# Kernel tuning notes

Measured on AMD Instinct MI355X. Metric: run time of the kernel, lower is better.

## Reference

```python
import jax, jax.numpy as jnp
import numpy as np

DIM = 256
NUM_HEADS = 8
HEAD_DIM = 64
NUM_MEM_KV = 4
HIDDEN = NUM_HEADS * HEAD_DIM  # 512


def rmsnorm(x, g):
    # F.normalize(x, dim=1) * g * sqrt(C)
    c = x.shape[1]
    n = jnp.sqrt(jnp.sum(x * x, axis=1, keepdims=True))
    xn = x / jnp.maximum(n, 1e-12)
    return xn * g * (c ** 0.5)


def setup_inputs() -> dict:
    key = jax.random.key(0)
    ks = jax.random.split(key, 7)
    b, h, w = 16, 64, 64
    x = jax.random.normal(ks[0], (b, DIM, h, w), dtype=jnp.float32)
    g_in = jnp.ones((1, DIM, 1, 1), dtype=jnp.float32)
    w_qkv = jax.random.normal(ks[1], (HIDDEN * 3, DIM), dtype=jnp.float32) * (1.0 / np.sqrt(DIM))
    mem_kv = jax.random.normal(ks[2], (2, NUM_HEADS, HEAD_DIM, NUM_MEM_KV), dtype=jnp.float32)
    w_out = jax.random.normal(ks[3], (DIM, HIDDEN), dtype=jnp.float32) * (1.0 / np.sqrt(HIDDEN))
    b_out = jax.random.normal(ks[4], (DIM,), dtype=jnp.float32) * 0.01
    g_out = jnp.ones((1, DIM, 1, 1), dtype=jnp.float32)
    return {"x": x, "g_in": g_in, "w_qkv": w_qkv, "mem_kv": mem_kv,
            "w_out": w_out, "b_out": b_out, "g_out": g_out}


def reference(x, g_in, w_qkv, mem_kv, w_out, b_out, g_out):
    b, c, h, w = x.shape
    scale = HEAD_DIM ** (-0.5)
    xn = rmsnorm(x, g_in)
    # 1x1 conv (no bias) as GEMM: [b, 3*hidden, h, w]
    qkv = jnp.einsum('bcxy,oc->boxy', xn, w_qkv)
    q, k, v = jnp.split(qkv, 3, axis=1)
    # b (heads d) x y -> b heads d n
    def to_heads(t):
        return t.reshape(b, NUM_HEADS, HEAD_DIM, h * w)
    q, k, v = to_heads(q), to_heads(k), to_heads(v)
    mem_k = jnp.broadcast_to(mem_kv[0], (b, NUM_HEADS, HEAD_DIM, NUM_MEM_KV))
    mem_v = jnp.broadcast_to(mem_kv[1], (b, NUM_HEADS, HEAD_DIM, NUM_MEM_KV))
    k = jnp.concatenate([mem_k, k], axis=-1)
    v = jnp.concatenate([mem_v, v], axis=-1)
    q = jax.nn.softmax(q, axis=-2) * scale   # softmax over head_dim
    k = jax.nn.softmax(k, axis=-1)           # softmax over sequence
    context = jnp.einsum('bhdn,bhen->bhde', k, v)  # [b,h,d,d] per-head context
    out = jnp.einsum('bhde,bhdn->bhen', context, q)  # [b,h,d,n]
    out = out.reshape(b, HIDDEN, h, w)
    out = jnp.einsum('bcxy,oc->boxy', out, w_out) + b_out[None, :, None, None]
    return rmsnorm(out, g_out)
```

## Files before the change

kernel.cpp:

```cpp
#include <hip/hip_runtime.h>
#include <hip/hip_bf16.h>

typedef __hip_bfloat16 bf16;
typedef short bf16x8 __attribute__((ext_vector_type(8)));
typedef float f32x4 __attribute__((ext_vector_type(4)));

#define PTOT  65536
#define NPOS  4096
#define CIN   256
#define HID   512
#define HD    64

__device__ __forceinline__ float us2f(unsigned short u) {
    return __uint_as_float(((unsigned int)u) << 16);
}
__device__ __forceinline__ float ldf(const void* p, size_t i, bool bf) {
    return bf ? us2f(((const unsigned short*)p)[i]) : ((const float*)p)[i];
}
__device__ __forceinline__ unsigned short f2bs(float v) {
    __hip_bfloat16 h = __float2bfloat16(v);
    return *reinterpret_cast<unsigned short*>(&h);
}
__device__ __forceinline__ void gld16(const void* g, void* s) {
    __builtin_amdgcn_global_load_lds(
        (const __attribute__((address_space(1))) unsigned int*)g,
        (__attribute__((address_space(3))) unsigned int*)s, 16, 0, 0);
}

__global__ __launch_bounds__(256) void k_detect(const unsigned* __restrict__ x,
                                                int* __restrict__ flag) {
    int t = threadIdx.x;
    unsigned w = x[(size_t)t * 997];
    unsigned e7 = (w >> 8) & 0x7f;
    __shared__ int s[256];
    s[t] = (e7 >= 58 && e7 <= 66) ? 1 : 0;
    __syncthreads();
    for (int k = 128; k > 0; k >>= 1) { if (t < k) s[t] += s[t + k]; __syncthreads(); }
    if (t == 0) flag[0] = (s[0] >= 128) ? 1 : 0;
}

__global__ void k_relay(const int* __restrict__ src, int* __restrict__ dst) {
    dst[0] = src[0];
}

__global__ __launch_bounds__(256) void k_cvt(const void* __restrict__ src,
        unsigned short* __restrict__ dst, int n, const int* __restrict__ flag) {
    bool bf = flag[0] != 0;
    int i = blockIdx.x * 256 + threadIdx.x;
    if (i < n) dst[i] = f2bs(ldf(src, i, bf));
}

template<bool BF>
__device__ __forceinline__ void norm_xn_body(const void* __restrict__ x,
        const void* __restrict__ g, unsigned short* __restrict__ xn,
        float* __restrict__ smem)
{
    float* xs   = smem;
    float* gS   = smem + 17216;
    float* red2 = smem + 17472;
    float* sS   = smem + 18496;
    const int t = threadIdx.x;
    const int p0 = blockIdx.x * 64;
    const int b = p0 >> 12;
    const int posbase = p0 & 4095;
    gS[t] = ldf(g, t, BF);
    __syncthreads();
    const int pl4 = (t & 15) * 4;
    const int crow = t >> 4;
    const size_t xbase = ((size_t)b * CIN) << 12;
    float ssq[4] = {0.f, 0.f, 0.f, 0.f};
    #pragma unroll
    for (int rr = 0; rr < 16; ++rr) {
        int c = rr * 16 + crow;
        float v[4];
        if (BF) {
            ushort4 u = *(const ushort4*)((const unsigned short*)x + xbase +
                                          ((size_t)c << 12) + posbase + pl4);
            v[0] = us2f(u.x); v[1] = us2f(u.y); v[2] = us2f(u.z); v[3] = us2f(u.w);
        } else {
            float4 f = *(const float4*)((const float*)x + xbase +
                                        ((size_t)c << 12) + posbase + pl4);
            v[0] = f.x; v[1] = f.y; v[2] = f.z; v[3] = f.w;
        }
        float gv = gS[c];
        float* row = xs + (c >> 6) * 4304 + (c & 63) * 67;
        #pragma unroll
        for (int e = 0; e < 4; ++e) {
            ssq[e] += v[e] * v[e];
            row[pl4 + e] = v[e] * gv;
        }
    }
    #pragma unroll
    for (int e = 0; e < 4; ++e) red2[crow * 64 + pl4 + e] = ssq[e];
    __syncthreads();
    if (t < 64) {
        float tot = 0.f;
        #pragma unroll
        for (int j = 0; j < 16; ++j) tot += red2[j * 64 + t];
        sS[t] = 16.0f / fmaxf(sqrtf(tot), 1e-12f);
    }
    __syncthreads();
    const int pr = t >> 2, c0 = (t & 3) * 64;
    const float sc = sS[pr];
    const float* base = xs + (t & 3) * 4304 + pr;
    unsigned short* dst = &xn[(size_t)(p0 + pr) * 256 + c0];
    #pragma unroll
    for (int q = 0; q < 4; ++q) {
        unsigned short tmp[16];
        #pragma unroll
        for (int j = 0; j < 16; ++j)
            tmp[j] = f2bs(base[(q * 16 + j) * 67] * sc);
        *(uint4*)(dst + q * 16)     = ((uint4*)tmp)[0];
        *(uint4*)(dst + q * 16 + 8) = ((uint4*)tmp)[1];
    }
}
__global__ __launch_bounds__(256) void k_norm_xn(
        const void* __restrict__ x, const void* __restrict__ g,
        unsigned short* __restrict__ xn, const int* __restrict__ flag)
{
    __shared__ float smem[18560];
    if (flag[0]) norm_xn_body<true>(x, g, xn, smem);
    else         norm_xn_body<false>(x, g, xn, smem);
}

template<int KTOT, bool BIAS, int OSTRIDE>
__global__ __launch_bounds__(256) void k_mfma(
        const bf16* __restrict__ Am, const bf16* __restrict__ Bm,
        const void* __restrict__ bias, bf16* __restrict__ C,
        const int* __restrict__ flag)
{
    __shared__ __align__(16) unsigned short As[128 * 32];
    __shared__ __align__(16) unsigned short Bs[128 * 32];
    const int tid = threadIdx.x;
    const int wv = tid >> 6, lane = tid & 63;
    const int quad = lane >> 4, l16 = lane & 15;
    const int wm = wv >> 1, wn = wv & 1;
    const int m0 = blockIdx.y * 128, n0 = blockIdx.x * 128;
    f32x4 acc[4][4] = {};
    const bf16* gA = Am + (size_t)(m0 + (tid >> 2)) * KTOT + (tid & 3) * 8;
    const bf16* gB = Bm + (size_t)(n0 + (tid >> 2)) * KTOT + (tid & 3) * 8;
    unsigned short* lA = As + wv * 512;
    unsigned short* lB = Bs + wv * 512;
    for (int k0 = 0; k0 < KTOT; k0 += 32) {
        gld16(gA + k0, lA);
        gld16(gA + (size_t)64 * KTOT + k0, lA + 2048);
        gld16(gB + k0, lB);
        gld16(gB + (size_t)64 * KTOT + k0, lB + 2048);
        __syncthreads();
        bf16x8 bfr[4];
        #pragma unroll
        for (int j = 0; j < 4; ++j)
            bfr[j] = *(const bf16x8*)&Bs[(wn * 64 + j * 16 + l16) * 32 + quad * 8];
        #pragma unroll
        for (int i = 0; i < 4; ++i) {
            bf16x8 af = *(const bf16x8*)&As[(wm * 64 + i * 16 + l16) * 32 + quad * 8];
            #pragma unroll
            for (int j = 0; j < 4; ++j)
                acc[i][j] = __builtin_amdgcn_mfma_f32_16x16x32_bf16(af, bfr[j], acc[i][j], 0, 0, 0);
        }
        __syncthreads();
    }
    bool bf = BIAS ? (flag[0] != 0) : false;
    #pragma unroll
    for (int i = 0; i < 4; ++i) {
        int row = m0 + wm * 64 + i * 16 + quad * 4;
        #pragma unroll
        for (int r = 0; r < 4; ++r) {
            float bv = BIAS ? ldf(bias, row + r, bf) : 0.0f;
            #pragma unroll
            for (int j = 0; j < 4; ++j) {
                int col = n0 + wn * 64 + j * 16 + l16;
                C[(size_t)(row + r) * OSTRIDE + col] = __float2bfloat16(acc[i][j][r] + bv);
            }
        }
    }
}

__global__ __launch_bounds__(512) void k_kvgemm(
        const bf16* __restrict__ Am, const bf16* __restrict__ Bm,
        bf16* __restrict__ C)
{
    __shared__ __align__(16) unsigned short As[128 * 256];
    __shared__ __align__(16) unsigned short Bs[2][64 * 256];
    const int t = threadIdx.x;
    const int w = t >> 6, lane = t & 63;
    const int quad = lane >> 4, l16 = lane & 15;
    const int wm = w >> 1, wn = w & 1;
    const int p = blockIdx.x;
    const int xcd = p & 7, slot = p >> 3;
    const int chunk = xcd * 4 + (slot & 3);
    const int mt = slot >> 2;
    const int m0 = mt * 128;
    const size_t cbase = (size_t)chunk * 2048;

    const int srow = t >> 5;
    const int sks  = (t & 31) ^ (srow & 7);

    #pragma unroll
    for (int q = 0; q < 8; ++q)
        gld16(Am + (size_t)(m0 + q * 16 + srow) * 256 + sks * 8,
              (char*)As + q * 8192 + w * 1024);
    #pragma unroll
    for (int q = 0; q < 4; ++q)
        gld16(Bm + (cbase + q * 16 + srow) * 256 + sks * 8,
              (char*)Bs[0] + q * 8192 + w * 1024);
    #pragma unroll
    for (int q = 0; q < 4; ++q)
        gld16(Bm + (cbase + 64 + q * 16 + srow) * 256 + sks * 8,
              (char*)Bs[1] + q * 8192 + w * 1024);

    asm volatile("s_waitcnt vmcnt(8)" ::: "memory");
    __builtin_amdgcn_s_barrier();
    asm volatile("" ::: "memory");

    bf16x8 af[2][8];
    #pragma unroll
    for (int i = 0; i < 2; ++i) {
        int row = wm * 32 + i * 16 + l16;
        #pragma unroll
        for (int kk = 0; kk < 8; ++kk)
            af[i][kk] = *(const bf16x8*)((const char*)As + row * 512 +
                         (((kk * 4 + quad) ^ (row & 7)) << 4));
    }

    for (int s = 0; s < 32; ++s) {
        if (s > 0) {
            asm volatile("" ::: "memory");
            __builtin_amdgcn_s_barrier();
            asm volatile("" ::: "memory");
            if (s + 1 < 32) {
                #pragma unroll
                for (int q = 0; q < 4; ++q)
                    gld16(Bm + (cbase + (size_t)(s + 1) * 64 + q * 16 + srow) * 256 + sks * 8,
                          (char*)Bs[(s + 1) & 1] + q * 8192 + w * 1024);
            }
        }
        if (s == 0)      asm volatile("s_waitcnt vmcnt(4)"  ::: "memory");
        else if (s < 31) asm volatile("s_waitcnt vmcnt(20)" ::: "memory");
        else             asm volatile("s_waitcnt vmcnt(16)" ::: "memory");
        __builtin_amdgcn_s_barrier();
        asm volatile("" ::: "memory");

        const unsigned short* Bbuf = Bs[s & 1];
        f32x4 acc[2][2] = {};
        #pragma unroll
        for (int kk = 0; kk < 8; ++kk) {
            bf16x8 bfr[2];
            #pragma unroll
            for (int j = 0; j < 2; ++j) {
                int row = wn * 32 + j * 16 + l16;
                bfr[j] = *(const bf16x8*)((const char*)Bbuf + row * 512 +
                          (((kk * 4 + quad) ^ (row & 7)) << 4));
            }
            #pragma unroll
            for (int i = 0; i < 2; ++i)
                #pragma unroll
                for (int j = 0; j < 2; ++j)
                    acc[i][j] = __builtin_amdgcn_mfma_f32_16x16x32_bf16(af[i][kk], bfr[j], acc[i][j], 0, 0, 0);
        }
        #pragma unroll
        for (int i = 0; i < 2; ++i) {
            #pragma unroll
            for (int r = 0; r < 4; ++r) {
                int row = m0 + wm * 32 + i * 16 + quad * 4 + r;
                size_t col = cbase + (size_t)s * 64 + wn * 32;
                #pragma unroll
                for (int j = 0; j < 2; ++j)
                    C[(size_t)row * PTOT + col + j * 16 + l16] = __float2bfloat16(acc[i][j][r]);
            }
        }
    }
}

__global__ __launch_bounds__(512, 2) void k_qapply(
        const bf16* __restrict__ xn, const bf16* __restrict__ wq,
        const unsigned short* __restrict__ ct_bf,
        unsigned short* __restrict__ oat_pe)
{
    __shared__ __align__(16) char smem[163840];
    const int t = threadIdx.x;
    const int w = t >> 6, lane = t & 63;
    const int quad = lane >> 4, l16 = lane & 15;
    const int wm = w >> 1, wn = w & 1;
    const int bid = blockIdx.x;
    const int hp = (bid >> 3) & 3;
    const int c  = (bid & 7) | ((bid >> 5) << 3);
    const int n0 = hp * 128;
    const size_t P0 = (size_t)c * 1024;
    const int b = c >> 2;
    const int srow = t >> 5, sks = (t & 31) ^ (srow & 7);

    #pragma unroll
    for (int k = 0; k < 2; ++k) {
        int u = k * 512 + t;
        int hh = u >> 9, rem = u & 511, e = rem >> 3, sl = rem & 7;
        gld16(ct_bf + (size_t)(b * 8 + hp * 2 + hh) * 4096 + e * 64 + ((sl ^ (e & 7)) * 8),
              smem + 81920 + k * 8192 + w * 1024);
    }
    #pragma unroll
    for (int q = 0; q < 8; ++q)
        gld16(wq + (size_t)(n0 + q * 16 + srow) * 256 + sks * 8,
              smem + q * 8192 + w * 1024);
    #pragma unroll
    for (int q = 0; q < 4; ++q)
        gld16(xn + (P0 + q * 16 + srow) * 256 + sks * 8,
              smem + 98304 + q * 8192 + w * 1024);
    #pragma unroll
    for (int q = 0; q < 4; ++q)
        gld16(xn + (P0 + 64 + q * 16 + srow) * 256 + sks * 8,
              smem + 131072 + q * 8192 + w * 1024);

    asm volatile("s_waitcnt vmcnt(8)" ::: "memory");
    __builtin_amdgcn_s_barrier();
    asm volatile("" ::: "memory");

    bf16x8 wqf[4][8];
    #pragma unroll
    for (int j = 0; j < 4; ++j) {
        int row = wn * 64 + j * 16 + l16;
        #pragma unroll
        for (int kk = 0; kk < 8; ++kk)
            wqf[j][kk] = *(const bf16x8*)(smem + row * 512 +
                          (((kk * 4 + quad) ^ (row & 7)) << 4));
    }

    unsigned short* qsm = (unsigned short*)(smem + 65536);

    for (int s = 0; s < 16; ++s) {
        if (s > 0) {
            asm volatile("" ::: "memory");
            __builtin_amdgcn_s_barrier();
            asm volatile("" ::: "memory");
            if (s + 1 < 16) {
                #pragma unroll
                for (int q = 0; q < 4; ++q)
                    gld16(xn + (P0 + (size_t)(s + 1) * 64 + q * 16 + srow) * 256 + sks * 8,
                          smem + 98304 + ((s + 1) & 1) * 32768 + q * 8192 + w * 1024);
            }
        }
        if (s == 0)      asm volatile("s_waitcnt vmcnt(4)"  ::: "memory");
        else if (s < 15) asm volatile("s_waitcnt vmcnt(20)" ::: "memory");
        else             asm volatile("s_waitcnt vmcnt(16)" ::: "memory");
        __builtin_amdgcn_s_barrier();
        asm volatile("" ::: "memory");

        const char* Bbuf = smem + 98304 + (s & 1) * 32768;
        f32x4 acc[4] = {};
        #pragma unroll
        for (int kk = 0; kk < 8; ++kk) {
            int row = wm * 16 + l16;
            bf16x8 xf = *(const bf16x8*)(Bbuf + row * 512 +
                          (((kk * 4 + quad) ^ (row & 7)) << 4));
            #pragma unroll
            for (int j = 0; j < 4; ++j)
                acc[j] = __builtin_amdgcn_mfma_f32_16x16x32_bf16(xf, wqf[j][kk], acc[j], 0, 0, 0);
        }

        #pragma unroll
        for (int r = 0; r < 4; ++r) {
            float m = fmaxf(fmaxf(acc[0][r], acc[1][r]), fmaxf(acc[2][r], acc[3][r]));
            m = fmaxf(m, __shfl_xor(m, 1));
            m = fmaxf(m, __shfl_xor(m, 2));
            m = fmaxf(m, __shfl_xor(m, 4));
            m = fmaxf(m, __shfl_xor(m, 8));
            float ev[4], sum = 0.f;
            #pragma unroll
            for (int j = 0; j < 4; ++j) { ev[j] = __expf(acc[j][r] - m); sum += ev[j]; }
            sum += __shfl_xor(sum, 1);
            sum += __shfl_xor(sum, 2);
            sum += __shfl_xor(sum, 4);
            sum += __shfl_xor(sum, 8);
            float inv = 0.125f / sum;
            int pos = wm * 16 + quad * 4 + r;
            #pragma unroll
            for (int j = 0; j < 4; ++j) {
                int ch = wn * 64 + j * 16 + l16;
                qsm[pos * 128 + (((ch >> 3) ^ (pos & 7)) << 3) + (ch & 7)] = f2bs(ev[j] * inv);
            }
        }

        f32x4 acc2[4] = {};
        #pragma unroll
        for (int kk = 0; kk < 2; ++kk) {
            int row = wm * 16 + l16;
            bf16x8 qf = *(const bf16x8*)(smem + 65536 + row * 256 +
                         (((wn * 8 + kk * 4 + quad) ^ (row & 7)) << 4));
            #pragma unroll
            for (int j = 0; j < 4; ++j) {
                int e = j * 16 + l16;
                bf16x8 cf = *(const bf16x8*)(smem + 81920 + wn * 8192 + e * 128 +
                             (((kk * 4 + quad) ^ (e & 7)) << 4));
                acc2[j] = __builtin_amdgcn_mfma_f32_16x16x32_bf16(qf, cf, acc2[j], 0, 0, 0);
            }
        }
        #pragma unroll
        for (int j = 0; j < 4; ++j)
            #pragma unroll
            for (int r = 0; r < 4; ++r) {
                size_t prow = P0 + (size_t)s * 64 + wm * 16 + quad * 4 + r;
                oat_pe[prow * HID + n0 + wn * 64 + j * 16 + l16] = f2bs(acc2[j][r]);
            }
    }
}

__global__ __launch_bounds__(256) void k_kstats(
        const bf16* __restrict__ kv, const void* __restrict__ memkv,
        float* __restrict__ rowmax, float* __restrict__ rowinv,
        const int* __restrict__ flag)
{
    bool bf = flag[0] != 0;
    int r = blockIdx.x;
    int b = r >> 9, hd = r & 511;
    const unsigned short* krow = (const unsigned short*)kv + (size_t)hd * PTOT + b * NPOS;
    int t = threadIdx.x;
    float vals[16];
    float m = -1e30f;
    #pragma unroll
    for (int i = 0; i < 16; ++i) {
        vals[i] = us2f(krow[t + (i << 8)]);
        m = fmaxf(m, vals[i]);
    }
    float mv = (t < 4) ? ldf(memkv, hd * 4 + t, bf) : -1e30f;
    m = fmaxf(m, mv);
    __shared__ float red[256];
    red[t] = m; __syncthreads();
    for (int s = 128; s > 0; s >>= 1) {
        if (t < s) red[t] = fmaxf(red[t], red[t + s]);
        __syncthreads();
    }
    float M = red[0]; __syncthreads();
    float sum = 0.f;
    #pragma unroll
    for (int i = 0; i < 16; ++i) sum += __expf(vals[i] - M);
    if (t < 4) sum += __expf(mv - M);
    red[t] = sum; __syncthreads();
    for (int s = 128; s > 0; s >>= 1) {
        if (t < s) red[t] += red[t + s];
        __syncthreads();
    }
    if (t == 0) { rowmax[r] = M; rowinv[r] = 1.0f / red[0]; }
}

__global__ __launch_bounds__(256) void k_context_mfma(
        const bf16* __restrict__ kv, const void* __restrict__ memkv,
        const float* __restrict__ rowmax, const float* __restrict__ rowinv,
        float* __restrict__ ctpart, const int* __restrict__ flag)
{
    bool bf = flag[0] != 0;
    int bh = blockIdx.x, chunk = blockIdx.y;
    int b = bh >> 3, h = bh & 7;
    __shared__ __align__(16) unsigned short As[4][64 * 32];
    __shared__ __align__(16) unsigned short Bs[4][64 * 32];
    __shared__ float rmS[64], riS[64];
    const int tid = threadIdx.x;
    if (tid < 64) {
        rmS[tid] = rowmax[(b << 9) + (h << 6) + tid];
        riS[tid] = rowinv[(b << 9) + (h << 6) + tid];
    }
    __syncthreads();
    const int wv = tid >> 6, lane = tid & 63;
    const int quad = lane >> 4, l16 = lane & 15;
    const int wm = wv >> 1, wn = wv & 1;
    const int krow = tid >> 2, kseg = tid & 3;
    const float rm = rmS[krow], ri = riS[krow];
    const unsigned short* kbase = (const unsigned short*)kv + (size_t)(h * HD) * PTOT + b * NPOS + chunk * 1024;
    const unsigned short* vbase = (const unsigned short*)kv + (size_t)(HID + h * HD) * PTOT + b * NPOS + chunk * 1024;
    f32x4 acc[2][2] = {};
    for (int s = 0; s < 8; ++s) {
        int nb = s * 128;
        #pragma unroll
        for (int kk = 0; kk < 4; ++kk) {
            uint4 u = *(const uint4*)(kbase + (size_t)krow * PTOT + nb + kk * 32 + kseg * 8);
            unsigned short out[8];
            const unsigned short* us = (const unsigned short*)&u;
            #pragma unroll
            for (int e = 0; e < 8; ++e)
                out[e] = f2bs(__expf(us2f(us[e]) - rm) * ri);
            *(uint4*)&As[kk][krow * 32 + kseg * 8] = *(uint4*)out;
        }
        #pragma unroll
        for (int kk = 0; kk < 4; ++kk)
            gld16(vbase + (size_t)(wv * 16 + (lane >> 2)) * PTOT + nb + kk * 32 + (lane & 3) * 8,
                  &Bs[kk][wv * 512]);
        __syncthreads();
        #pragma unroll
        for (int kk = 0; kk < 4; ++kk) {
            bf16x8 bfr[2];
            #pragma unroll
            for (int j = 0; j < 2; ++j)
                bfr[j] = *(const bf16x8*)&Bs[kk][(wn * 32 + j * 16 + l16) * 32 + quad * 8];
            #pragma unroll
            for (int i = 0; i < 2; ++i) {
                bf16x8 af = *(const bf16x8*)&As[kk][(wm * 32 + i * 16 + l16) * 32 + quad * 8];
                #pragma unroll
                for (int j = 0; j < 2; ++j)
                    acc[i][j] = __builtin_amdgcn_mfma_f32_16x16x32_bf16(af, bfr[j], acc[i][j], 0, 0, 0);
            }
        }
        __syncthreads();
    }
    if (chunk == 0) {
        float mv[2][4];
        #pragma unroll
        for (int j = 0; j < 2; ++j) {
            int e = wn * 32 + j * 16 + l16;
            #pragma unroll
            for (int mm = 0; mm < 4; ++mm)
                mv[j][mm] = ldf(memkv, 2048 + ((h << 6) + e) * 4 + mm, bf);
        }
        #pragma unroll
        for (int i = 0; i < 2; ++i) {
            #pragma unroll
            for (int r = 0; r < 4; ++r) {
                int d = wm * 32 + i * 16 + quad * 4 + r;
                #pragma unroll
                for (int mm = 0; mm < 4; ++mm) {
                    float kw = __expf(ldf(memkv, ((h << 6) + d) * 4 + mm, bf) - rmS[d]) * riS[d];
                    #pragma unroll
                    for (int j = 0; j < 2; ++j)
                        acc[i][j][r] = fmaf(kw, mv[j][mm], acc[i][j][r]);
                }
            }
        }
    }
    float* outp = ctpart + (size_t)(chunk * 128 + bh) * 4096;
    #pragma unroll
    for (int i = 0; i < 2; ++i) {
        #pragma unroll
        for (int r = 0; r < 4; ++r) {
            int d = wm * 32 + i * 16 + quad * 4 + r;
            #pragma unroll
            for (int j = 0; j < 2; ++j) {
                int e = wn * 32 + j * 16 + l16;
                outp[d * 64 + e] = acc[i][j][r];
            }
        }
    }
}

__global__ __launch_bounds__(256) void k_ctsum(
        const float* __restrict__ ctpart, unsigned short* __restrict__ ct_bf)
{
    int bh = blockIdx.x, t = threadIdx.x;
    int i0 = t * 16;
    int e = i0 >> 6, d0 = i0 & 63;
    unsigned short tmp[16];
    #pragma unroll
    for (int j = 0; j < 16; ++j) {
        int d = d0 + j;
        float s = 0.f;
        #pragma unroll
        for (int c = 0; c < 4; ++c)
            s += ctpart[(size_t)(c * 128 + bh) * 4096 + d * 64 + e];
        tmp[j] = f2bs(s);
    }
    unsigned short* dst = ct_bf + (size_t)bh * 4096 + i0;
    *(uint4*)dst = ((uint4*)tmp)[0];
    *(uint4*)(dst + 8) = ((uint4*)tmp)[1];
}

template<bool BF>
__device__ __forceinline__ void rmsout_body(const unsigned short* __restrict__ pre,
        const void* __restrict__ g, void* __restrict__ out, float* __restrict__ smem)
{
    float* gS   = smem;
    float* red2 = smem + 256;
    float* sS   = smem + 1280;
    const int t = threadIdx.x;
    const int p0 = blockIdx.x * 64;
    const int b = p0 >> 12;
    const int posbase = p0 & 4095;
    gS[t] = ldf(g, t, BF);
    const int pl4 = (t & 15) * 4;
    const int crow = t >> 4;
    const unsigned short* pbase = pre + p0 + pl4;
    ushort4 u[16];
    float ssq[4] = {0.f, 0.f, 0.f, 0.f};
    #pragma unroll
    for (int rr = 0; rr < 16; ++rr) {
        int c = rr * 16 + crow;
        u[rr] = *(const ushort4*)(pbase + (size_t)c * PTOT);
        float v0 = us2f(u[rr].x), v1 = us2f(u[rr].y), v2 = us2f(u[rr].z), v3 = us2f(u[rr].w);
        ssq[0] += v0 * v0; ssq[1] += v1 * v1; ssq[2] += v2 * v2; ssq[3] += v3 * v3;
    }
    #pragma unroll
    for (int e = 0; e < 4; ++e) red2[crow * 64 + pl4 + e] = ssq[e];
    __syncthreads();
    if (t < 64) {
        float tot = 0.f;
        #pragma unroll
        for (int j = 0; j < 16; ++j) tot += red2[j * 64 + t];
        sS[t] = 16.0f / fmaxf(sqrtf(tot), 1e-12f);
    }
    __syncthreads();
    const float s0 = sS[pl4], s1 = sS[pl4 + 1], s2 = sS[pl4 + 2], s3 = sS[pl4 + 3];
    #pragma unroll
    for (int rr = 0; rr < 16; ++rr) {
        int c = rr * 16 + crow;
        float gv = gS[c];
        float v0 = us2f(u[rr].x) * s0 * gv;
        float v1 = us2f(u[rr].y) * s1 * gv;
        float v2 = us2f(u[rr].z) * s2 * gv;
        float v3 = us2f(u[rr].w) * s3 * gv;
        size_t oi = ((size_t)(b * CIN + c) << 12) + posbase + pl4;
        if (BF) {
            ushort4 o;
            o.x = f2bs(v0); o.y = f2bs(v1); o.z = f2bs(v2); o.w = f2bs(v3);
            *(ushort4*)((unsigned short*)out + oi) = o;
        } else {
            float4 o; o.x = v0; o.y = v1; o.z = v2; o.w = v3;
            *(float4*)((float*)out + oi) = o;
        }
    }
}
__global__ __launch_bounds__(256) void k_rmsnorm_out(
        const unsigned short* __restrict__ pre, const void* __restrict__ g,
        void* __restrict__ out, const int* __restrict__ flag)
{
    __shared__ float smem[1344];
    if (flag[0]) rmsout_body<true>(pre, g, out, smem);
    else         rmsout_body<false>(pre, g, out, smem);
}

extern "C" void kernel_launch(void* const* d_in, const int* in_sizes, int n_in,
                              void* d_out, int out_size, void* d_ws, size_t ws_size,
                              hipStream_t stream) {
    const void* x     = d_in[0];
    const void* g_in  = d_in[1];
    const void* w_qkv = d_in[2];
    const void* memkv = d_in[3];
    const void* w_out = d_in[4];
    const void* b_out = d_in[5];
    const void* g_out = d_in[6];

    char* ws = (char*)d_ws;
    bf16*           kv     = (bf16*)ws;
    unsigned short* oat_pe = (unsigned short*)(ws + 67108864);
    unsigned short* pre    = (unsigned short*)ws;
    int*            flagB  = (int*)(ws + 50331648);

    char* ob = (char*)d_out;
    float*          ctpart = (float*)ob;
    float*          rowmax = (float*)(ob + 8388608);
    float*          rowinv = (float*)(ob + 8421376);
    int*            flagA  = (int*)(ob + 8454144);
    unsigned short* wq_b   = (unsigned short*)(ob + 9437184);
    unsigned short* wout_b = (unsigned short*)(ob + 10485760);
    unsigned short* ct_bf  = (unsigned short*)(ob + 11010048);
    unsigned short* xn     = (unsigned short*)(ob + 12582912);

    k_detect<<<1, 256, 0, stream>>>((const unsigned*)x, flagA);

    k_cvt<<<1536, 256, 0, stream>>>(w_qkv, wq_b, 1536 * 256, flagA);
    k_cvt<<<512, 256, 0, stream>>>(w_out, wout_b, 256 * 512, flagA);

    k_norm_xn<<<1024, 256, 0, stream>>>(x, g_in, xn, flagA);

    k_kvgemm<<<256, 512, 0, stream>>>(
        (const bf16*)(wq_b + (size_t)512 * CIN), (const bf16*)xn, kv);

    k_kstats<<<8192, 256, 0, stream>>>(kv, memkv, rowmax, rowinv, flagA);

    dim3 gctx(128, 4);
    k_context_mfma<<<gctx, 256, 0, stream>>>(kv, memkv, rowmax, rowinv, ctpart, flagA);

    k_ctsum<<<128, 256, 0, stream>>>(ctpart, ct_bf);

    k_qapply<<<256, 512, 0, stream>>>(
        (const bf16*)xn, (const bf16*)wq_b, ct_bf, oat_pe);

    dim3 go(512, 2);
    k_mfma<HID, true, PTOT><<<go, 256, 0, stream>>>(
        (const bf16*)wout_b, (const bf16*)oat_pe, b_out, (bf16*)pre, flagA);

    k_relay<<<1, 1, 0, stream>>>(flagA, flagB);

    k_rmsnorm_out<<<1024, 256, 0, stream>>>(pre, g_out, d_out, flagB);
}
```

Measured before the change: 329.7 us.

## Alias A and B LDS buffers in kv GEMM and double the grid

```diff
diff --git a/kernel.cpp b/kernel.cpp
--- a/kernel.cpp
+++ b/kernel.cpp
@@ -176,22 +176,20 @@
     }
 }
 
-__global__ __launch_bounds__(512) void k_kvgemm(
+__global__ __launch_bounds__(512, 4) void k_kvgemm(
         const bf16* __restrict__ Am, const bf16* __restrict__ Bm,
         bf16* __restrict__ C)
 {
-    __shared__ __align__(16) unsigned short As[128 * 256];
-    __shared__ __align__(16) unsigned short Bs[2][64 * 256];
+    __shared__ __align__(16) char smem[65536];
     const int t = threadIdx.x;
     const int w = t >> 6, lane = t & 63;
     const int quad = lane >> 4, l16 = lane & 15;
     const int wm = w >> 1, wn = w & 1;
-    const int p = blockIdx.x;
-    const int xcd = p & 7, slot = p >> 3;
-    const int chunk = xcd * 4 + (slot & 3);
-    const int mt = slot >> 2;
+    const int bid = blockIdx.x;
+    const int c  = (bid & 7) | ((bid >> 6) << 3);
+    const int mt = (bid >> 3) & 7;
     const int m0 = mt * 128;
-    const size_t cbase = (size_t)chunk * 2048;
+    const size_t cbase = (size_t)c * 1024;
 
     const int srow = t >> 5;
     const int sks  = (t & 31) ^ (srow & 7);
@@ -199,49 +197,52 @@
     #pragma unroll
     for (int q = 0; q < 8; ++q)
         gld16(Am + (size_t)(m0 + q * 16 + srow) * 256 + sks * 8,
-              (char*)As + q * 8192 + w * 1024);
+              smem + q * 8192 + w * 1024);
+    asm volatile("s_waitcnt vmcnt(0)" ::: "memory");
+    __builtin_amdgcn_s_barrier();
+    asm volatile("" ::: "memory");
+
+    bf16x8 af[2][8];
+    #pragma unroll
+    for (int i = 0; i < 2; ++i) {
+        int row = wm * 32 + i * 16 + l16;
+        #pragma unroll
+        for (int kk = 0; kk < 8; ++kk)
+            af[i][kk] = *(const bf16x8*)(smem + row * 512 +
+                         (((kk * 4 + quad) ^ (row & 7)) << 4));
+    }
+    asm volatile("s_waitcnt lgkmcnt(0)" ::: "memory");
+    __builtin_amdgcn_s_barrier();
+    asm volatile("" ::: "memory");
+
     #pragma unroll
     for (int q = 0; q < 4; ++q)
         gld16(Bm + (cbase + q * 16 + srow) * 256 + sks * 8,
-              (char*)Bs[0] + q * 8192 + w * 1024);
+              smem + q * 8192 + w * 1024);
     #pragma unroll
     for (int q = 0; q < 4; ++q)
         gld16(Bm + (cbase + 64 + q * 16 + srow) * 256 + sks * 8,
-              (char*)Bs[1] + q * 8192 + w * 1024);
-
-    asm volatile("s_waitcnt vmcnt(8)" ::: "memory");
-    __builtin_amdgcn_s_barrier();
-    asm volatile("" ::: "memory");
-
-    bf16x8 af[2][8];
-    #pragma unroll
-    for (int i = 0; i < 2; ++i) {
-        int row = wm * 32 + i * 16 + l16;
-        #pragma unroll
-        for (int kk = 0; kk < 8; ++kk)
-            af[i][kk] = *(const bf16x8*)((const char*)As + row * 512 +
-                         (((kk * 4 + quad) ^ (row & 7)) << 4));
-    }
-
-    for (int s = 0; s < 32; ++s) {
+              smem + 32768 + q * 8192 + w * 1024);
+
+    for (int s = 0; s < 16; ++s) {
         if (s > 0) {
             asm volatile("" ::: "memory");
             __builtin_amdgcn_s_barrier();
             asm volatile("" ::: "memory");
-            if (s + 1 < 32) {
+            if (s + 1 < 16) {
                 #pragma unroll
                 for (int q = 0; q < 4; ++q)
                     gld16(Bm + (cbase + (size_t)(s + 1) * 64 + q * 16 + srow) * 256 + sks * 8,
-                          (char*)Bs[(s + 1) & 1] + q * 8192 + w * 1024);
+                          smem + ((s + 1) & 1) * 32768 + q * 8192 + w * 1024);
             }
         }
         if (s == 0)      asm volatile("s_waitcnt vmcnt(4)"  ::: "memory");
-        else if (s < 31) asm volatile("s_waitcnt vmcnt(20)" ::: "memory");
+        else if (s < 15) asm volatile("s_waitcnt vmcnt(20)" ::: "memory");
         else             asm volatile("s_waitcnt vmcnt(16)" ::: "memory");
         __builtin_amdgcn_s_barrier();
         asm volatile("" ::: "memory");
 
-        const unsigned short* Bbuf = Bs[s & 1];
+        const char* Bbuf = smem + (s & 1) * 32768;
         f32x4 acc[2][2] = {};
         #pragma unroll
         for (int kk = 0; kk < 8; ++kk) {
@@ -249,7 +250,7 @@
             #pragma unroll
             for (int j = 0; j < 2; ++j) {
                 int row = wn * 32 + j * 16 + l16;
-                bfr[j] = *(const bf16x8*)((const char*)Bbuf + row * 512 +
+                bfr[j] = *(const bf16x8*)(Bbuf + row * 512 +
                           (((kk * 4 + quad) ^ (row & 7)) << 4));
             }
             #pragma unroll
@@ -656,7 +657,7 @@
 
     k_norm_xn<<<1024, 256, 0, stream>>>(x, g_in, xn, flagA);
 
-    k_kvgemm<<<256, 512, 0, stream>>>(
+    k_kvgemm<<<512, 512, 0, stream>>>(
         (const bf16*)(wq_b + (size_t)512 * CIN), (const bf16*)xn, kv);
 
     k_kstats<<<8192, 256, 0, stream>>>(kv, memkv, rowmax, rowinv, flagA);
```

Measured after the change: 318.7 us. -3.4%, faster.
